# Optimization experiments

Measured on AMD Instinct MI355X. Metric: run time of the kernel, lower is better.

The kernel has to match this reference:

```python
import jax, jax.numpy as jnp
import numpy as np

RADIUS = 0.05
HMIN = -0.02
HMAXES = (0.01, 0.02, 0.03, 0.04)
NSAMPLE = 64
BN_EPS = 1e-5


def _group(d_rot, hmax):
    # d_rot: (B,S,N,3) seed-relative coords rotated into the gripper frame (d @ R)
    # Cylinder query: approach axis is x; keep first NSAMPLE points with
    # y^2+z^2 < r^2 and hmin < x < hmax; pad with first hit (0 if no hit),
    # matching the CUDA cylinder_query kernel semantics.
    N = d_rot.shape[2]
    h = d_rot[..., 0]
    r2 = d_rot[..., 1] ** 2 + d_rot[..., 2] ** 2
    mask = (r2 < RADIUS * RADIUS) & (h > HMIN) & (h < hmax)
    key = jnp.where(mask, jnp.arange(N, dtype=jnp.int32), N)
    neg_top, _ = jax.lax.top_k(-key, NSAMPLE)   # ascending keys = first hits in point order
    idx = -neg_top                               # (B,S,k); == N where slot is invalid
    first = idx[..., :1]
    idx = jnp.where(idx < N, idx, jnp.where(first < N, first, 0))
    return jnp.take_along_axis(d_rot, idx[..., None], axis=2)  # (B,S,k,3)


def _mlp_layer(x, w, b, g, be, m, v):
    # 1x1 Conv2d + BatchNorm (eval-mode, running stats) + ReLU, as in pt_utils.SharedMLP
    x = jnp.einsum('bcpn,oc->bopn', x, w) + b[None, :, None, None]
    scale = g / jnp.sqrt(v + BN_EPS)
    x = (x - m[None, :, None, None]) * scale[None, :, None, None] + be[None, :, None, None]
    return jax.nn.relu(x)


def _forward(seed_xyz, pointcloud, vp_rot, params):
    B, S, _ = seed_xyz.shape
    D = len(HMAXES)
    d = pointcloud[:, None, :, :] - seed_xyz[:, :, None, :]          # (B,S,N,3)
    d_rot = jnp.einsum('bsnc,bscd->bsnd', d, vp_rot)                 # rotate into gripper frame
    groups = jnp.stack([_group(d_rot, h) for h in HMAXES], axis=2)   # (B,S,D,k,3)
    x = groups.transpose(0, 4, 1, 2, 3).reshape(B, 3, S * D, NSAMPLE)  # (B,3,S*D,k)
    for (w, b, g, be, m, v) in params:
        x = _mlp_layer(x, w, b, g, be, m, v)
    x = x.max(axis=-1)                                               # max-pool over nsample
    return x.reshape(B, -1, S, D)                                    # (B,256,S,D)


def setup_inputs() -> dict:
    key = jax.random.key(0)
    ks = jax.random.split(key, 8)
    B, S, N = 2, 1024, 16384
    inp = {
        'seed_xyz': jax.random.uniform(ks[0], (B, S, 3), jnp.float32),
        'pointcloud': jax.random.uniform(ks[1], (B, N, 3), jnp.float32),
        'vp_rot': jax.random.normal(ks[2], (B, S, 3, 3), jnp.float32),
    }
    dims = [3, 64, 128, 256]
    for i in range(3):
        cin, cout = dims[i], dims[i + 1]
        k1, k2, k3, k4, k5, k6 = jax.random.split(ks[3 + i], 6)
        inp[f'w{i+1}'] = jax.random.normal(k1, (cout, cin), jnp.float32) * 0.05
        inp[f'b{i+1}'] = jax.random.normal(k2, (cout,), jnp.float32) * 0.01
        inp[f'g{i+1}'] = 1.0 + 0.1 * jax.random.normal(k3, (cout,), jnp.float32)
        inp[f'be{i+1}'] = jax.random.normal(k4, (cout,), jnp.float32) * 0.01
        inp[f'm{i+1}'] = jax.random.normal(k5, (cout,), jnp.float32) * 0.01
        inp[f'v{i+1}'] = jax.random.uniform(k6, (cout,), jnp.float32, 0.5, 1.5)
    return inp


def reference(seed_xyz, pointcloud, vp_rot,
              w1, b1, g1, be1, m1, v1,
              w2, b2, g2, be2, m2, v2,
              w3, b3, g3, be3, m3, v3):
    params = [(w1, b1, g1, be1, m1, v1),
              (w2, b2, g2, be2, m2, v2),
              (w3, b3, g3, be3, m3, v3)]
    return _forward(seed_xyz, pointcloud, vp_rot, params)
```

## Files before the change

kernel.cpp:

```cpp
#include <hip/hip_runtime.h>
#include <hip/hip_bf16.h>
#include <cstdint>
#include <cstddef>

#define NSAMP  64
#define NPT    16384
#define NLVL   4
#define NCHUNK 8
#define CHSZ   (NPT / NCHUNK)

typedef __attribute__((ext_vector_type(8))) short  short8;
typedef __attribute__((ext_vector_type(4))) float  floatx4;
typedef __attribute__((ext_vector_type(4))) unsigned int uintx4;
typedef __attribute__((ext_vector_type(2))) unsigned int uintx2;

__device__ __forceinline__ unsigned short f2bf(float x) {
    union { float f; unsigned int u; } c; c.f = x;
    unsigned int r = (c.u + 0x7fffu + ((c.u >> 16) & 1u)) >> 16;
    return (unsigned short)r;
}
__device__ __forceinline__ unsigned int f2bf2(float a, float b) {
    __hip_bfloat162 t = __float22bfloat162_rn(make_float2(a, b));
    union { __hip_bfloat162 h; unsigned int u; } c; c.h = t;
    return c.u;
}

__global__ __launch_bounds__(256) void prep_kernel(
    const float* __restrict__ w1, const float* __restrict__ b1, const float* __restrict__ g1,
    const float* __restrict__ be1, const float* __restrict__ m1, const float* __restrict__ v1,
    const float* __restrict__ w2, const float* __restrict__ b2, const float* __restrict__ g2,
    const float* __restrict__ be2, const float* __restrict__ m2, const float* __restrict__ v2,
    const float* __restrict__ w3, const float* __restrict__ b3, const float* __restrict__ g3,
    const float* __restrict__ be3, const float* __restrict__ m3, const float* __restrict__ v3,
    float* __restrict__ w1f, float* __restrict__ fb1,
    unsigned short* __restrict__ w2b, float* __restrict__ fb2,
    unsigned short* __restrict__ w3b, float* __restrict__ fb3)
{
    const int t  = blockIdx.x * 256 + threadIdx.x;
    const int nt = gridDim.x * 256;
    const float eps = 1e-5f;
    for (int i = t; i < 64 * 3; i += nt)    w1f[i] = w1[i] * (g1[i / 3] / sqrtf(v1[i / 3] + eps));
    for (int i = t; i < 64; i += nt)        fb1[i] = (b1[i] - m1[i]) * (g1[i] / sqrtf(v1[i] + eps)) + be1[i];
    for (int i = t; i < 128 * 64; i += nt)  w2b[i] = f2bf(w2[i] * (g2[i / 64] / sqrtf(v2[i / 64] + eps)));
    for (int i = t; i < 128; i += nt)       fb2[i] = (b2[i] - m2[i]) * (g2[i] / sqrtf(v2[i] + eps)) + be2[i];
    for (int i = t; i < 256 * 128; i += nt) w3b[i] = f2bf(w3[i] * (g3[i / 128] / sqrtf(v3[i / 128] + eps)));
    for (int i = t; i < 256; i += nt)       fb3[i] = (b3[i] - m3[i]) * (g3[i] / sqrtf(v3[i] + eps)) + be3[i];
}

__global__ __launch_bounds__(512) void scan_kernel(
    const float* __restrict__ seedp, const float* __restrict__ pc,
    const float* __restrict__ rot, unsigned short* __restrict__ buf,
    int* __restrict__ cnts)
{
    __shared__ float ch[CHSZ * 3];
    const int tid  = threadIdx.x;
    const int lane = tid & 63;
    const int w    = tid >> 6;
    const int sg   = blockIdx.x >> 3;
    const int c    = blockIdx.x & 7;
    const int g    = sg * 8 + w;
    const int b    = g >> 10;

    {
        const float4* src = (const float4*)(pc + ((size_t)b * NPT + c * CHSZ) * 3);
        float4* dst = (float4*)ch;
        dst[tid]        = src[tid];
        dst[tid + 512]  = src[tid + 512];
        dst[tid + 1024] = src[tid + 1024];
    }
    __syncthreads();

    const float* sd = seedp + (size_t)g * 3;
    const float sx = sd[0], sy = sd[1], sz = sd[2];
    const float* R = rot + (size_t)g * 9;
    const float r00 = R[0], r01 = R[1], r02 = R[2];
    const float r10 = R[3], r11 = R[4], r12 = R[5];
    const float r20 = R[6], r21 = R[7], r22 = R[8];
    const float nc0 = -(sx * r00 + sy * r10 + sz * r20);
    const float nc1 = -(sx * r01 + sy * r11 + sz * r21);
    const float nc2 = -(sx * r02 + sy * r12 + sz * r22);

    unsigned short* bufg = buf + (size_t)g * (NLVL * NCHUNK * 64);
    int cnt0 = 0, cnt1 = 0, cnt2 = 0, cnt3 = 0;
    const unsigned long long lm = (1ull << lane) - 1ull;

    for (int bt = 0; bt < 4; ++bt) {
        float pxv[8], pyv[8], pzv[8];
        #pragma unroll
        for (int j = 0; j < 8; ++j) {
            const int pl = (bt * 8 + j) * 64 + lane;
            pxv[j] = ch[pl * 3];
            pyv[j] = ch[pl * 3 + 1];
            pzv[j] = ch[pl * 3 + 2];
        }
        #pragma unroll
        for (int j = 0; j < 8; ++j) {
            const float h = fmaf(pxv[j], r00, fmaf(pyv[j], r10, fmaf(pzv[j], r20, nc0)));
            const float u = fmaf(pxv[j], r01, fmaf(pyv[j], r11, fmaf(pzv[j], r21, nc1)));
            const float v = fmaf(pxv[j], r02, fmaf(pyv[j], r12, fmaf(pzv[j], r22, nc2)));
            const float r2 = fmaf(u, u, v * v);
            const bool base = (r2 < 0.0025f) && (h > -0.02f) && (h < 0.04f);

            const unsigned long long bal3 = __ballot(base);
            if (bal3 == 0ull) continue;

            const unsigned short pidx = (unsigned short)(c * CHSZ + (bt * 8 + j) * 64 + lane);
            #pragma unroll
            for (int l = 0; l < NLVL; ++l) {
                unsigned long long bal; bool m;
                if (l == 3) { m = base; bal = bal3; }
                else {
                    const float hm = (l == 0) ? 0.01f : (l == 1) ? 0.02f : 0.03f;
                    m = base && (h < hm);
                    bal = __ballot(m);
                }
                int& cnt = (l == 0) ? cnt0 : (l == 1) ? cnt1 : (l == 2) ? cnt2 : cnt3;
                if (m) {
                    const int pos = cnt + (int)__popcll(bal & lm);
                    if (pos < 64) bufg[(l * NCHUNK + c) * 64 + pos] = pidx;
                }
                cnt += (int)__popcll(bal);
            }
        }
        if (cnt0 >= NSAMP) break;
    }

    if (lane == 0) {
        int* cg = cnts + (size_t)g * (NLVL * NCHUNK);
        cg[0 * NCHUNK + c] = cnt0;
        cg[1 * NCHUNK + c] = cnt1;
        cg[2 * NCHUNK + c] = cnt2;
        cg[3 * NCHUNK + c] = cnt3;
    }
}

__global__ __launch_bounds__(256) void gather_kernel(
    const float* __restrict__ seedp, const float* __restrict__ pc,
    const float* __restrict__ rot,
    const unsigned short* __restrict__ buf, const int* __restrict__ cnts,
    float* __restrict__ gx)
{
    const int n = threadIdx.x & 63;
    const int W = blockIdx.x * 4 + (threadIdx.x >> 6);
    const int g = W >> 2, l = W & 3;
    const int b = g >> 10;

    const int* cg = cnts + (size_t)g * (NLVL * NCHUNK) + l * NCHUNK;
    const unsigned short* bl = buf + (size_t)g * (NLVL * NCHUNK * 64) + l * (NCHUNK * 64);
    int idx = -1, acc = 0, firstIdx = -1;
    #pragma unroll
    for (int c = 0; c < NCHUNK; ++c) {
        const int cn = min(cg[c], 64);
        if (cn > 0 && firstIdx < 0) firstIdx = (int)bl[c * 64];
        if (n >= acc && n < acc + cn) idx = (int)bl[c * 64 + (n - acc)];
        acc += cn;
    }
    if (idx < 0) idx = (firstIdx >= 0) ? firstIdx : 0;

    const float* sd = seedp + (size_t)g * 3;
    const float* R  = rot   + (size_t)g * 9;
    const float* pp = pc + ((size_t)b * NPT + idx) * 3;
    const float dx = pp[0] - sd[0], dy = pp[1] - sd[1], dz = pp[2] - sd[2];

    float* o = gx + (size_t)W * 192;
    o[n]       = dx * R[0] + dy * R[3] + dz * R[6];
    o[64 + n]  = dx * R[1] + dy * R[4] + dz * R[7];
    o[128 + n] = dx * R[2] + dy * R[5] + dz * R[8];
}

__global__ __launch_bounds__(256) void mlp_kernel(
    const float* __restrict__ gx, const int* __restrict__ cnts,
    const float* __restrict__ w1f, const float* __restrict__ fb1,
    const unsigned short* __restrict__ w2b, const float* __restrict__ fb2,
    const unsigned short* __restrict__ w3b, const float* __restrict__ fb3,
    float* __restrict__ out)
{
    __shared__ unsigned short h1t[4096];
    __shared__ unsigned short h2t[8192];

    const int tid = threadIdx.x;
    const int n      = tid & 63;
    const int w      = tid >> 6;
    const int lane15 = tid & 15;
    const int quad   = (tid & 63) >> 4;

    int fmask;
    {
        const int* cg0 = cnts + (size_t)blockIdx.x * (NLVL * NCHUNK);
        int fm = 0;
        #pragma unroll
        for (int l = 0; l < NLVL; ++l) {
            int kn = 0;
            #pragma unroll
            for (int c = 0; c < NCHUNK; ++c) kn += min(cg0[l * NCHUNK + c], 64);
            fm |= (kn <= 16) ? (1 << l) : 0;
        }
        fmask = __builtin_amdgcn_readfirstlane(fm);
    }

    short8 wa3[4][4];
    float  wb3[4];
    #pragma unroll
    for (int mt = 0; mt < 4; ++mt) {
        const int m0 = (w * 4 + mt) * 16;
        #pragma unroll
        for (int k0 = 0; k0 < 4; ++k0)
            wa3[mt][k0] = *(const short8*)&w3b[(m0 + lane15) * 128 + k0 * 32 + quad * 8];
        wb3[mt] = fb3[m0 + lane15];
    }

    short8 a20[2], a21[2]; floatx4 b2v[2];
    #pragma unroll
    for (int mi = 0; mi < 2; ++mi) {
        const int m0 = (w * 2 + mi) * 16;
        a20[mi] = *(const short8*)&w2b[(m0 + lane15) * 64 + quad * 8];
        a21[mi] = *(const short8*)&w2b[(m0 + lane15) * 64 + 32 + quad * 8];
        b2v[mi] = *(const floatx4*)&fb2[m0 + quad * 4];
    }

    if (fmask == 15) {
        const int gb = blockIdx.x;
        const int b = gb >> 10, s = gb & 1023;

        {
            const float* xb = gx + (size_t)(gb * 4 + (n >> 4)) * 192;
            const int sidx = n & 15;
            const float x0 = xb[sidx], x1 = xb[64 + sidx], x2 = xb[128 + sidx];
            unsigned int p[8];
            #pragma unroll
            for (int j = 0; j < 8; ++j) {
                const int o0 = __builtin_amdgcn_readfirstlane(w * 16 + 2 * j);
                const float a0 = fb1[o0]     + w1f[o0*3]*x0   + w1f[o0*3+1]*x1 + w1f[o0*3+2]*x2;
                const float a1 = fb1[o0 + 1] + w1f[o0*3+3]*x0 + w1f[o0*3+4]*x1 + w1f[o0*3+5]*x2;
                p[j] = f2bf2(fmaxf(a0, 0.f), fmaxf(a1, 0.f));
            }
            *(uintx4*)&h1t[(((w * 2)    ) * 64 + n) * 8] = (uintx4){p[0], p[1], p[2], p[3]};
            *(uintx4*)&h1t[(((w * 2) + 1) * 64 + n) * 8] = (uintx4){p[4], p[5], p[6], p[7]};
        }
        __syncthreads();

        {
            short8 bfr[4][2];
            #pragma unroll
            for (int nt = 0; nt < 4; ++nt)
                #pragma unroll
                for (int k0 = 0; k0 < 2; ++k0)
                    bfr[nt][k0] = *(const short8*)&h1t[((k0 * 4 + quad) * 64 + nt * 16 + lane15) * 8];

            #pragma unroll
            for (int mi = 0; mi < 2; ++mi) {
                const int m0 = (w * 2 + mi) * 16;
                #pragma unroll
                for (int nt = 0; nt < 4; ++nt) {
                    floatx4 acc = b2v[mi];
                    acc = __builtin_amdgcn_mfma_f32_16x16x32_bf16(a20[mi], bfr[nt][0], acc, 0, 0, 0);
                    acc = __builtin_amdgcn_mfma_f32_16x16x32_bf16(a21[mi], bfr[nt][1], acc, 0, 0, 0);
                    const int n2 = nt * 16 + lane15;
                    const unsigned int q0 = f2bf2(fmaxf(acc[0], 0.f), fmaxf(acc[1], 0.f));
                    const unsigned int q1 = f2bf2(fmaxf(acc[2], 0.f), fmaxf(acc[3], 0.f));
                    const int kb = (m0 >> 3) + (quad >> 1);
                    *(uintx2*)&h2t[(kb * 64 + n2) * 8 + (quad & 1) * 4] = (uintx2){q0, q1};
                }
            }
        }
        __syncthreads();

        short8 bfr3[4][4];
        #pragma unroll
        for (int nt = 0; nt < 4; ++nt)
            #pragma unroll
            for (int k0 = 0; k0 < 4; ++k0)
                bfr3[nt][k0] = *(const short8*)&h2t[((k0 * 4 + quad) * 64 + nt * 16 + lane15) * 8];

        #pragma unroll
        for (int mt = 0; mt < 4; ++mt) {
            floatx4 acc[4];
            #pragma unroll
            for (int nt = 0; nt < 4; ++nt) acc[nt] = (floatx4){0.f, 0.f, 0.f, 0.f};
            #pragma unroll
            for (int k0 = 0; k0 < 4; ++k0)
                #pragma unroll
                for (int nt = 0; nt < 4; ++nt)
                    acc[nt] = __builtin_amdgcn_mfma_f32_16x16x32_bf16(bfr3[nt][k0], wa3[mt][k0], acc[nt], 0, 0, 0);

            float tv[4];
            #pragma unroll
            for (int nt = 0; nt < 4; ++nt) {
                float t = fmaxf(fmaxf(acc[nt][0], acc[nt][1]), fmaxf(acc[nt][2], acc[nt][3]));
                t = fmaxf(t, __shfl_xor(t, 16));
                t = fmaxf(t, __shfl_xor(t, 32));
                tv[nt] = fmaxf(t + wb3[mt], 0.f);
            }
            if (quad == 0) {
                const int o = (w * 4 + mt) * 16 + lane15;
                *(float4*)&out[(((size_t)b * 256 + o) * 1024 + s) * 4] =
                    make_float4(tv[0], tv[1], tv[2], tv[3]);
            }
        }
        return;
    }

    {
        const float* xb = gx + (size_t)(blockIdx.x * 4) * 192;
        const float x0 = xb[n], x1 = xb[64 + n], x2 = xb[128 + n];
        unsigned int p[8];
        #pragma unroll
        for (int j = 0; j < 8; ++j) {
            const int o0 = __builtin_amdgcn_readfirstlane(w * 16 + 2 * j);
            const float a0 = fb1[o0]     + w1f[o0*3]*x0   + w1f[o0*3+1]*x1 + w1f[o0*3+2]*x2;
            const float a1 = fb1[o0 + 1] + w1f[o0*3+3]*x0 + w1f[o0*3+4]*x1 + w1f[o0*3+5]*x2;
            p[j] = f2bf2(fmaxf(a0, 0.f), fmaxf(a1, 0.f));
        }
        *(uintx4*)&h1t[(((w * 2)    ) * 64 + n) * 8] = (uintx4){p[0], p[1], p[2], p[3]};
        *(uintx4*)&h1t[(((w * 2) + 1) * 64 + n) * 8] = (uintx4){p[4], p[5], p[6], p[7]};
    }

    for (int it = 0; it < 4; ++it) {
        const int gp = blockIdx.x * 4 + it;
        const int g = gp >> 2, l = gp & 3;
        const int b = g >> 10, s = g & 1023;
        const bool fastit = (fmask >> it) & 1;

        __syncthreads();

        if (fastit) {
            const short8 bA = *(const short8*)&h1t[((0 * 4 + quad) * 64 + lane15) * 8];
            const short8 bB = *(const short8*)&h1t[((1 * 4 + quad) * 64 + lane15) * 8];
            #pragma unroll
            for (int mi = 0; mi < 2; ++mi) {
                floatx4 acc = b2v[mi];
                acc = __builtin_amdgcn_mfma_f32_16x16x32_bf16(a20[mi], bA, acc, 0, 0, 0);
                acc = __builtin_amdgcn_mfma_f32_16x16x32_bf16(a21[mi], bB, acc, 0, 0, 0);
                const unsigned int q0 = f2bf2(fmaxf(acc[0], 0.f), fmaxf(acc[1], 0.f));
                const unsigned int q1 = f2bf2(fmaxf(acc[2], 0.f), fmaxf(acc[3], 0.f));
                const int kb = (w * 2 + mi) * 2 + (quad >> 1);
                *(uintx2*)&h2t[(kb * 64 + lane15) * 8 + (quad & 1) * 4] = (uintx2){q0, q1};
            }
        } else {
            short8 bfr[4][2];
            #pragma unroll
            for (int nt = 0; nt < 4; ++nt)
                #pragma unroll
                for (int k0 = 0; k0 < 2; ++k0)
                    bfr[nt][k0] = *(const short8*)&h1t[((k0 * 4 + quad) * 64 + nt * 16 + lane15) * 8];

            #pragma unroll
            for (int mi = 0; mi < 2; ++mi) {
                const int m0 = (w * 2 + mi) * 16;
                #pragma unroll
                for (int nt = 0; nt < 4; ++nt) {
                    floatx4 acc = b2v[mi];
                    acc = __builtin_amdgcn_mfma_f32_16x16x32_bf16(a20[mi], bfr[nt][0], acc, 0, 0, 0);
                    acc = __builtin_amdgcn_mfma_f32_16x16x32_bf16(a21[mi], bfr[nt][1], acc, 0, 0, 0);
                    const int n2 = nt * 16 + lane15;
                    const unsigned int q0 = f2bf2(fmaxf(acc[0], 0.f), fmaxf(acc[1], 0.f));
                    const unsigned int q1 = f2bf2(fmaxf(acc[2], 0.f), fmaxf(acc[3], 0.f));
                    const int kb = (m0 >> 3) + (quad >> 1);
                    *(uintx2*)&h2t[(kb * 64 + n2) * 8 + (quad & 1) * 4] = (uintx2){q0, q1};
                }
            }
        }
        __syncthreads();

        if (fastit) {
            short8 bf3[4];
            #pragma unroll
            for (int k0 = 0; k0 < 4; ++k0)
                bf3[k0] = *(const short8*)&h2t[((k0 * 4 + quad) * 64 + lane15) * 8];

            if (it < 3) {
                const float* xb = gx + (size_t)(gp + 1) * 192;
                const float x0 = xb[n], x1 = xb[64 + n], x2 = xb[128 + n];
                unsigned int p[8];
                #pragma unroll
                for (int j = 0; j < 8; ++j) {
                    const int o0 = __builtin_amdgcn_readfirstlane(w * 16 + 2 * j);
                    const float a0 = fb1[o0]     + w1f[o0*3]*x0   + w1f[o0*3+1]*x1 + w1f[o0*3+2]*x2;
                    const float a1 = fb1[o0 + 1] + w1f[o0*3+3]*x0 + w1f[o0*3+4]*x1 + w1f[o0*3+5]*x2;
                    p[j] = f2bf2(fmaxf(a0, 0.f), fmaxf(a1, 0.f));
                }
                *(uintx4*)&h1t[(((w * 2)    ) * 64 + n) * 8] = (uintx4){p[0], p[1], p[2], p[3]};
                *(uintx4*)&h1t[(((w * 2) + 1) * 64 + n) * 8] = (uintx4){p[4], p[5], p[6], p[7]};
            }

            #pragma unroll
            for (int mt = 0; mt < 4; ++mt) {
                floatx4 acc = (floatx4){0.f, 0.f, 0.f, 0.f};
                #pragma unroll
                for (int k0 = 0; k0 < 4; ++k0)
                    acc = __builtin_amdgcn_mfma_f32_16x16x32_bf16(bf3[k0], wa3[mt][k0], acc, 0, 0, 0);

                float t = fmaxf(fmaxf(acc[0], acc[1]), fmaxf(acc[2], acc[3]));
                t = fmaxf(t, __shfl_xor(t, 16));
                t = fmaxf(t, __shfl_xor(t, 32));
                if (quad == 0) {
                    const int o = (w * 4 + mt) * 16 + lane15;
                    out[(((size_t)b * 256 + o) * 1024 + s) * 4 + l] = fmaxf(t + wb3[mt], 0.f);
                }
            }
        } else {
            short8 bfr3[4][4];
            #pragma unroll
            for (int nt = 0; nt < 4; ++nt)
                #pragma unroll
                for (int k0 = 0; k0 < 4; ++k0)
                    bfr3[nt][k0] = *(const short8*)&h2t[((k0 * 4 + quad) * 64 + nt * 16 + lane15) * 8];

            if (it < 3) {
                const float* xb = gx + (size_t)(gp + 1) * 192;
                const float x0 = xb[n], x1 = xb[64 + n], x2 = xb[128 + n];
                unsigned int p[8];
                #pragma unroll
                for (int j = 0; j < 8; ++j) {
                    const int o0 = __builtin_amdgcn_readfirstlane(w * 16 + 2 * j);
                    const float a0 = fb1[o0]     + w1f[o0*3]*x0   + w1f[o0*3+1]*x1 + w1f[o0*3+2]*x2;
                    const float a1 = fb1[o0 + 1] + w1f[o0*3+3]*x0 + w1f[o0*3+4]*x1 + w1f[o0*3+5]*x2;
                    p[j] = f2bf2(fmaxf(a0, 0.f), fmaxf(a1, 0.f));
                }
                *(uintx4*)&h1t[(((w * 2)    ) * 64 + n) * 8] = (uintx4){p[0], p[1], p[2], p[3]};
                *(uintx4*)&h1t[(((w * 2) + 1) * 64 + n) * 8] = (uintx4){p[4], p[5], p[6], p[7]};
            }

            #pragma unroll
            for (int mt = 0; mt < 4; ++mt) {
                floatx4 acc[4];
                #pragma unroll
                for (int nt = 0; nt < 4; ++nt) acc[nt] = (floatx4){0.f, 0.f, 0.f, 0.f};
                #pragma unroll
                for (int k0 = 0; k0 < 4; ++k0)
                    #pragma unroll
                    for (int nt = 0; nt < 4; ++nt)
                        acc[nt] = __builtin_amdgcn_mfma_f32_16x16x32_bf16(bfr3[nt][k0], wa3[mt][k0], acc[nt], 0, 0, 0);

                float t0 = fmaxf(fmaxf(acc[0][0], acc[0][1]), fmaxf(acc[0][2], acc[0][3]));
                float t1 = fmaxf(fmaxf(acc[1][0], acc[1][1]), fmaxf(acc[1][2], acc[1][3]));
                float t2 = fmaxf(fmaxf(acc[2][0], acc[2][1]), fmaxf(acc[2][2], acc[2][3]));
                float t3 = fmaxf(fmaxf(acc[3][0], acc[3][1]), fmaxf(acc[3][2], acc[3][3]));
                float t  = fmaxf(fmaxf(t0, t1), fmaxf(t2, t3));
                t = fmaxf(t, __shfl_xor(t, 16));
                t = fmaxf(t, __shfl_xor(t, 32));
                if (quad == 0) {
                    const int o = (w * 4 + mt) * 16 + lane15;
                    out[(((size_t)b * 256 + o) * 1024 + s) * 4 + l] = fmaxf(t + wb3[mt], 0.f);
                }
            }
        }
    }
}

extern "C" void kernel_launch(void* const* d_in, const int* in_sizes, int n_in,
                              void* d_out, int out_size, void* d_ws, size_t ws_size,
                              hipStream_t stream) {
    const float* seed = (const float*)d_in[0];
    const float* pc   = (const float*)d_in[1];
    const float* rot  = (const float*)d_in[2];
    const float* w1 = (const float*)d_in[3];
    const float* b1 = (const float*)d_in[4];
    const float* g1 = (const float*)d_in[5];
    const float* be1 = (const float*)d_in[6];
    const float* m1 = (const float*)d_in[7];
    const float* v1 = (const float*)d_in[8];
    const float* w2 = (const float*)d_in[9];
    const float* b2 = (const float*)d_in[10];
    const float* g2 = (const float*)d_in[11];
    const float* be2 = (const float*)d_in[12];
    const float* m2 = (const float*)d_in[13];
    const float* v2 = (const float*)d_in[14];
    const float* w3 = (const float*)d_in[15];
    const float* b3 = (const float*)d_in[16];
    const float* g3 = (const float*)d_in[17];
    const float* be3 = (const float*)d_in[18];
    const float* m3 = (const float*)d_in[19];
    const float* v3 = (const float*)d_in[20];

    float* w1f = (float*)d_ws;
    float* fb1 = w1f + 192;
    float* fb2 = fb1 + 64;
    float* fb3 = fb2 + 128;
    unsigned short* w2b = (unsigned short*)(fb3 + 256);
    unsigned short* w3b = w2b + 8192;
    unsigned short* buf = w3b + 32768;
    int* cnts = (int*)(buf + 4194304);
    float* gx = (float*)(cnts + 65536);

    prep_kernel<<<64, 256, 0, stream>>>(w1, b1, g1, be1, m1, v1,
                                        w2, b2, g2, be2, m2, v2,
                                        w3, b3, g3, be3, m3, v3,
                                        w1f, fb1, w2b, fb2, w3b, fb3);
    scan_kernel<<<2048, 512, 0, stream>>>(seed, pc, rot, buf, cnts);
    gather_kernel<<<2048, 256, 0, stream>>>(seed, pc, rot, buf, cnts, gx);
    mlp_kernel<<<2048, 256, 0, stream>>>(gx, cnts, w1f, fb1, w2b, fb2, w3b, fb3,
                                         (float*)d_out);
}
```

Baseline: 168.5 us.

## Fold weight prep into scan kernel and split MLP work by group occupancy

Measured after the change: 177.3 us. +5.2%, slower.

```diff
diff --git a/kernel.cpp b/kernel.cpp
--- a/kernel.cpp
+++ b/kernel.cpp
@@ -25,7 +25,10 @@
     return c.u;
 }
 
-__global__ __launch_bounds__(256) void prep_kernel(
+__global__ __launch_bounds__(512) void scan_kernel(
+    const float* __restrict__ seedp, const float* __restrict__ pc,
+    const float* __restrict__ rot, unsigned short* __restrict__ buf,
+    int* __restrict__ cnts,
     const float* __restrict__ w1, const float* __restrict__ b1, const float* __restrict__ g1,
     const float* __restrict__ be1, const float* __restrict__ m1, const float* __restrict__ v1,
     const float* __restrict__ w2, const float* __restrict__ b2, const float* __restrict__ g2,
@@ -36,24 +39,22 @@
     unsigned short* __restrict__ w2b, float* __restrict__ fb2,
     unsigned short* __restrict__ w3b, float* __restrict__ fb3)
 {
-    const int t  = blockIdx.x * 256 + threadIdx.x;
-    const int nt = gridDim.x * 256;
-    const float eps = 1e-5f;
-    for (int i = t; i < 64 * 3; i += nt)    w1f[i] = w1[i] * (g1[i / 3] / sqrtf(v1[i / 3] + eps));
-    for (int i = t; i < 64; i += nt)        fb1[i] = (b1[i] - m1[i]) * (g1[i] / sqrtf(v1[i] + eps)) + be1[i];
-    for (int i = t; i < 128 * 64; i += nt)  w2b[i] = f2bf(w2[i] * (g2[i / 64] / sqrtf(v2[i / 64] + eps)));
-    for (int i = t; i < 128; i += nt)       fb2[i] = (b2[i] - m2[i]) * (g2[i] / sqrtf(v2[i] + eps)) + be2[i];
-    for (int i = t; i < 256 * 128; i += nt) w3b[i] = f2bf(w3[i] * (g3[i / 128] / sqrtf(v3[i / 128] + eps)));
-    for (int i = t; i < 256; i += nt)       fb3[i] = (b3[i] - m3[i]) * (g3[i] / sqrtf(v3[i] + eps)) + be3[i];
-}
-
-__global__ __launch_bounds__(512) void scan_kernel(
-    const float* __restrict__ seedp, const float* __restrict__ pc,
-    const float* __restrict__ rot, unsigned short* __restrict__ buf,
-    int* __restrict__ cnts)
-{
     __shared__ float ch[CHSZ * 3];
     const int tid  = threadIdx.x;
+
+    if (blockIdx.x >= 2048) {
+        const int t  = (blockIdx.x - 2048) * 512 + tid;
+        const int nt = 64 * 512;
+        const float eps = 1e-5f;
+        for (int i = t; i < 64 * 3; i += nt)    w1f[i] = w1[i] * (g1[i / 3] / sqrtf(v1[i / 3] + eps));
+        for (int i = t; i < 64; i += nt)        fb1[i] = (b1[i] - m1[i]) * (g1[i] / sqrtf(v1[i] + eps)) + be1[i];
+        for (int i = t; i < 128 * 64; i += nt)  w2b[i] = f2bf(w2[i] * (g2[i / 64] / sqrtf(v2[i / 64] + eps)));
+        for (int i = t; i < 128; i += nt)       fb2[i] = (b2[i] - m2[i]) * (g2[i] / sqrtf(v2[i] + eps)) + be2[i];
+        for (int i = t; i < 256 * 128; i += nt) w3b[i] = f2bf(w3[i] * (g3[i / 128] / sqrtf(v3[i / 128] + eps)));
+        for (int i = t; i < 256; i += nt)       fb3[i] = (b3[i] - m3[i]) * (g3[i] / sqrtf(v3[i] + eps)) + be3[i];
+        return;
+    }
+
     const int lane = tid & 63;
     const int w    = tid >> 6;
     const int sg   = blockIdx.x >> 3;
@@ -184,48 +185,42 @@
     const int lane15 = tid & 15;
     const int quad   = (tid & 63) >> 4;
 
-    int fmask;
-    {
-        const int* cg0 = cnts + (size_t)blockIdx.x * (NLVL * NCHUNK);
-        int fm = 0;
-        #pragma unroll
-        for (int l = 0; l < NLVL; ++l) {
+    const int bi = blockIdx.x;
+
+    if (bi < 8192) {
+        const int gp = bi;
+        const int g = gp >> 2, l = gp & 3;
+        {
+            const int* cg = cnts + (size_t)g * (NLVL * NCHUNK) + l * NCHUNK;
             int kn = 0;
             #pragma unroll
-            for (int c = 0; c < NCHUNK; ++c) kn += min(cg0[l * NCHUNK + c], 64);
-            fm |= (kn <= 16) ? (1 << l) : 0;
-        }
-        fmask = __builtin_amdgcn_readfirstlane(fm);
-    }
-
-    short8 wa3[4][4];
-    float  wb3[4];
-    #pragma unroll
-    for (int mt = 0; mt < 4; ++mt) {
-        const int m0 = (w * 4 + mt) * 16;
-        #pragma unroll
-        for (int k0 = 0; k0 < 4; ++k0)
-            wa3[mt][k0] = *(const short8*)&w3b[(m0 + lane15) * 128 + k0 * 32 + quad * 8];
-        wb3[mt] = fb3[m0 + lane15];
-    }
-
-    short8 a20[2], a21[2]; floatx4 b2v[2];
-    #pragma unroll
-    for (int mi = 0; mi < 2; ++mi) {
-        const int m0 = (w * 2 + mi) * 16;
-        a20[mi] = *(const short8*)&w2b[(m0 + lane15) * 64 + quad * 8];
-        a21[mi] = *(const short8*)&w2b[(m0 + lane15) * 64 + 32 + quad * 8];
-        b2v[mi] = *(const floatx4*)&fb2[m0 + quad * 4];
-    }
-
-    if (fmask == 15) {
-        const int gb = blockIdx.x;
-        const int b = gb >> 10, s = gb & 1023;
+            for (int c = 0; c < NCHUNK; ++c) kn += min(cg[c], 64);
+            if (__builtin_amdgcn_readfirstlane(kn) <= 16) return;
+        }
+        const int b = g >> 10, s = g & 1023;
+
+        short8 wa3[4][4];
+        float  wb3[4];
+        #pragma unroll
+        for (int mt = 0; mt < 4; ++mt) {
+            const int m0 = (w * 4 + mt) * 16;
+            #pragma unroll
+            for (int k0 = 0; k0 < 4; ++k0)
+                wa3[mt][k0] = *(const short8*)&w3b[(m0 + lane15) * 128 + k0 * 32 + quad * 8];
+            wb3[mt] = fb3[m0 + lane15];
+        }
+        short8 a20[2], a21[2]; floatx4 b2v[2];
+        #pragma unroll
+        for (int mi = 0; mi < 2; ++mi) {
+            const int m0 = (w * 2 + mi) * 16;
+            a20[mi] = *(const short8*)&w2b[(m0 + lane15) * 64 + quad * 8];
+            a21[mi] = *(const short8*)&w2b[(m0 + lane15) * 64 + 32 + quad * 8];
+            b2v[mi] = *(const floatx4*)&fb2[m0 + quad * 4];
+        }
 
         {
-            const float* xb = gx + (size_t)(gb * 4 + (n >> 4)) * 192;
-            const int sidx = n & 15;
-            const float x0 = xb[sidx], x1 = xb[64 + sidx], x2 = xb[128 + sidx];
+            const float* xb = gx + (size_t)gp * 192;
+            const float x0 = xb[n], x1 = xb[64 + n], x2 = xb[128 + n];
             unsigned int p[8];
             #pragma unroll
             for (int j = 0; j < 8; ++j) {
@@ -283,26 +278,63 @@
                 for (int nt = 0; nt < 4; ++nt)
                     acc[nt] = __builtin_amdgcn_mfma_f32_16x16x32_bf16(bfr3[nt][k0], wa3[mt][k0], acc[nt], 0, 0, 0);
 
-            float tv[4];
-            #pragma unroll
-            for (int nt = 0; nt < 4; ++nt) {
-                float t = fmaxf(fmaxf(acc[nt][0], acc[nt][1]), fmaxf(acc[nt][2], acc[nt][3]));
-                t = fmaxf(t, __shfl_xor(t, 16));
-                t = fmaxf(t, __shfl_xor(t, 32));
-                tv[nt] = fmaxf(t + wb3[mt], 0.f);
-            }
+            float t0 = fmaxf(fmaxf(acc[0][0], acc[0][1]), fmaxf(acc[0][2], acc[0][3]));
+            float t1 = fmaxf(fmaxf(acc[1][0], acc[1][1]), fmaxf(acc[1][2], acc[1][3]));
+            float t2 = fmaxf(fmaxf(acc[2][0], acc[2][1]), fmaxf(acc[2][2], acc[2][3]));
+            float t3 = fmaxf(fmaxf(acc[3][0], acc[3][1]), fmaxf(acc[3][2], acc[3][3]));
+            float t  = fmaxf(fmaxf(t0, t1), fmaxf(t2, t3));
+            t = fmaxf(t, __shfl_xor(t, 16));
+            t = fmaxf(t, __shfl_xor(t, 32));
             if (quad == 0) {
                 const int o = (w * 4 + mt) * 16 + lane15;
-                *(float4*)&out[(((size_t)b * 256 + o) * 1024 + s) * 4] =
-                    make_float4(tv[0], tv[1], tv[2], tv[3]);
+                out[(((size_t)b * 256 + o) * 1024 + s) * 4 + l] = fmaxf(t + wb3[mt], 0.f);
             }
         }
         return;
     }
 
+    const int gb = bi - 8192;
+    const int b = gb >> 10, s = gb & 1023;
+
+    int F;
     {
-        const float* xb = gx + (size_t)(blockIdx.x * 4) * 192;
-        const float x0 = xb[n], x1 = xb[64 + n], x2 = xb[128 + n];
+        const int* cg0 = cnts + (size_t)gb * (NLVL * NCHUNK);
+        int fm = 0;
+        #pragma unroll
+        for (int l = 0; l < NLVL; ++l) {
+            int kn = 0;
+            #pragma unroll
+            for (int c = 0; c < NCHUNK; ++c) kn += min(cg0[l * NCHUNK + c], 64);
+            fm += (kn <= 16) ? 1 : 0;
+        }
+        F = __builtin_amdgcn_readfirstlane(fm);
+    }
+    if (F == 0) return;
+
+    short8 wa3[4][4];
+    float  wb3[4];
+    #pragma unroll
+    for (int mt = 0; mt < 4; ++mt) {
+        const int m0 = (w * 4 + mt) * 16;
+        #pragma unroll
+        for (int k0 = 0; k0 < 4; ++k0)
+            wa3[mt][k0] = *(const short8*)&w3b[(m0 + lane15) * 128 + k0 * 32 + quad * 8];
+        wb3[mt] = fb3[m0 + lane15];
+    }
+    short8 a20[2], a21[2]; floatx4 b2v[2];
+    #pragma unroll
+    for (int mi = 0; mi < 2; ++mi) {
+        const int m0 = (w * 2 + mi) * 16;
+        a20[mi] = *(const short8*)&w2b[(m0 + lane15) * 64 + quad * 8];
+        a21[mi] = *(const short8*)&w2b[(m0 + lane15) * 64 + 32 + quad * 8];
+        b2v[mi] = *(const floatx4*)&fb2[m0 + quad * 4];
+    }
+
+    {
+        const int lvl = min(n >> 4, F - 1);
+        const float* xb = gx + (size_t)(gb * 4 + lvl) * 192;
+        const int sidx = n & 15;
+        const float x0 = xb[sidx], x1 = xb[64 + sidx], x2 = xb[128 + sidx];
         unsigned int p[8];
         #pragma unroll
         for (int j = 0; j < 8; ++j) {
@@ -314,135 +346,69 @@
         *(uintx4*)&h1t[(((w * 2)    ) * 64 + n) * 8] = (uintx4){p[0], p[1], p[2], p[3]};
         *(uintx4*)&h1t[(((w * 2) + 1) * 64 + n) * 8] = (uintx4){p[4], p[5], p[6], p[7]};
     }
-
-    for (int it = 0; it < 4; ++it) {
-        const int gp = blockIdx.x * 4 + it;
-        const int g = gp >> 2, l = gp & 3;
-        const int b = g >> 10, s = g & 1023;
-        const bool fastit = (fmask >> it) & 1;
-
-        __syncthreads();
-
-        if (fastit) {
-            const short8 bA = *(const short8*)&h1t[((0 * 4 + quad) * 64 + lane15) * 8];
-            const short8 bB = *(const short8*)&h1t[((1 * 4 + quad) * 64 + lane15) * 8];
-            #pragma unroll
-            for (int mi = 0; mi < 2; ++mi) {
+    __syncthreads();
+
+    {
+        short8 bfr[4][2];
+        #pragma unroll
+        for (int nt = 0; nt < 4; ++nt)
+            #pragma unroll
+            for (int k0 = 0; k0 < 2; ++k0)
+                bfr[nt][k0] = *(const short8*)&h1t[((k0 * 4 + quad) * 64 + nt * 16 + lane15) * 8];
+
+        #pragma unroll
+        for (int mi = 0; mi < 2; ++mi) {
+            const int m0 = (w * 2 + mi) * 16;
+            #pragma unroll
+            for (int nt = 0; nt < 4; ++nt) {
                 floatx4 acc = b2v[mi];
-                acc = __builtin_amdgcn_mfma_f32_16x16x32_bf16(a20[mi], bA, acc, 0, 0, 0);
-                acc = __builtin_amdgcn_mfma_f32_16x16x32_bf16(a21[mi], bB, acc, 0, 0, 0);
+                acc = __builtin_amdgcn_mfma_f32_16x16x32_bf16(a20[mi], bfr[nt][0], acc, 0, 0, 0);
+                acc = __builtin_amdgcn_mfma_f32_16x16x32_bf16(a21[mi], bfr[nt][1], acc, 0, 0, 0);
+                const int n2 = nt * 16 + lane15;
                 const unsigned int q0 = f2bf2(fmaxf(acc[0], 0.f), fmaxf(acc[1], 0.f));
                 const unsigned int q1 = f2bf2(fmaxf(acc[2], 0.f), fmaxf(acc[3], 0.f));
-                const int kb = (w * 2 + mi) * 2 + (quad >> 1);
-                *(uintx2*)&h2t[(kb * 64 + lane15) * 8 + (quad & 1) * 4] = (uintx2){q0, q1};
-            }
-        } else {
-            short8 bfr[4][2];
+                const int kb = (m0 >> 3) + (quad >> 1);
+                *(uintx2*)&h2t[(kb * 64 + n2) * 8 + (quad & 1) * 4] = (uintx2){q0, q1};
+            }
+        }
+    }
+    __syncthreads();
+
+    short8 bfr3[4][4];
+    #pragma unroll
+    for (int nt = 0; nt < 4; ++nt)
+        #pragma unroll
+        for (int k0 = 0; k0 < 4; ++k0)
+            bfr3[nt][k0] = *(const short8*)&h2t[((k0 * 4 + quad) * 64 + nt * 16 + lane15) * 8];
+
+    #pragma unroll
+    for (int mt = 0; mt < 4; ++mt) {
+        floatx4 acc[4];
+        #pragma unroll
+        for (int nt = 0; nt < 4; ++nt) acc[nt] = (floatx4){0.f, 0.f, 0.f, 0.f};
+        #pragma unroll
+        for (int k0 = 0; k0 < 4; ++k0)
             #pragma unroll
             for (int nt = 0; nt < 4; ++nt)
-                #pragma unroll
-                for (int k0 = 0; k0 < 2; ++k0)
-                    bfr[nt][k0] = *(const short8*)&h1t[((k0 * 4 + quad) * 64 + nt * 16 + lane15) * 8];
-
-            #pragma unroll
-            for (int mi = 0; mi < 2; ++mi) {
-                const int m0 = (w * 2 + mi) * 16;
-                #pragma unroll
-                for (int nt = 0; nt < 4; ++nt) {
-                    floatx4 acc = b2v[mi];
-                    acc = __builtin_amdgcn_mfma_f32_16x16x32_bf16(a20[mi], bfr[nt][0], acc, 0, 0, 0);
-                    acc = __builtin_amdgcn_mfma_f32_16x16x32_bf16(a21[mi], bfr[nt][1], acc, 0, 0, 0);
-                    const int n2 = nt * 16 + lane15;
-                    const unsigned int q0 = f2bf2(fmaxf(acc[0], 0.f), fmaxf(acc[1], 0.f));
-                    const unsigned int q1 = f2bf2(fmaxf(acc[2], 0.f), fmaxf(acc[3], 0.f));
-                    const int kb = (m0 >> 3) + (quad >> 1);
-                    *(uintx2*)&h2t[(kb * 64 + n2) * 8 + (quad & 1) * 4] = (uintx2){q0, q1};
-                }
-            }
-        }
-        __syncthreads();
-
-        if (fastit) {
-            short8 bf3[4];
-            #pragma unroll
-            for (int k0 = 0; k0 < 4; ++k0)
-                bf3[k0] = *(const short8*)&h2t[((k0 * 4 + quad) * 64 + lane15) * 8];
-
-            if (it < 3) {
-                const float* xb = gx + (size_t)(gp + 1) * 192;
-                const float x0 = xb[n], x1 = xb[64 + n], x2 = xb[128 + n];
-                unsigned int p[8];
-                #pragma unroll
-                for (int j = 0; j < 8; ++j) {
-                    const int o0 = __builtin_amdgcn_readfirstlane(w * 16 + 2 * j);
-                    const float a0 = fb1[o0]     + w1f[o0*3]*x0   + w1f[o0*3+1]*x1 + w1f[o0*3+2]*x2;
-                    const float a1 = fb1[o0 + 1] + w1f[o0*3+3]*x0 + w1f[o0*3+4]*x1 + w1f[o0*3+5]*x2;
-                    p[j] = f2bf2(fmaxf(a0, 0.f), fmaxf(a1, 0.f));
-                }
-                *(uintx4*)&h1t[(((w * 2)    ) * 64 + n) * 8] = (uintx4){p[0], p[1], p[2], p[3]};
-                *(uintx4*)&h1t[(((w * 2) + 1) * 64 + n) * 8] = (uintx4){p[4], p[5], p[6], p[7]};
-            }
-
-            #pragma unroll
-            for (int mt = 0; mt < 4; ++mt) {
-                floatx4 acc = (floatx4){0.f, 0.f, 0.f, 0.f};
-                #pragma unroll
-                for (int k0 = 0; k0 < 4; ++k0)
-                    acc = __builtin_amdgcn_mfma_f32_16x16x32_bf16(bf3[k0], wa3[mt][k0], acc, 0, 0, 0);
-
-                float t = fmaxf(fmaxf(acc[0], acc[1]), fmaxf(acc[2], acc[3]));
-                t = fmaxf(t, __shfl_xor(t, 16));
-                t = fmaxf(t, __shfl_xor(t, 32));
-                if (quad == 0) {
-                    const int o = (w * 4 + mt) * 16 + lane15;
-                    out[(((size_t)b * 256 + o) * 1024 + s) * 4 + l] = fmaxf(t + wb3[mt], 0.f);
-                }
-            }
-        } else {
-            short8 bfr3[4][4];
-            #pragma unroll
-            for (int nt = 0; nt < 4; ++nt)
-                #pragma unroll
-                for (int k0 = 0; k0 < 4; ++k0)
-                    bfr3[nt][k0] = *(const short8*)&h2t[((k0 * 4 + quad) * 64 + nt * 16 + lane15) * 8];
-
-            if (it < 3) {
-                const float* xb = gx + (size_t)(gp + 1) * 192;
-                const float x0 = xb[n], x1 = xb[64 + n], x2 = xb[128 + n];
-                unsigned int p[8];
-                #pragma unroll
-                for (int j = 0; j < 8; ++j) {
-                    const int o0 = __builtin_amdgcn_readfirstlane(w * 16 + 2 * j);
-                    const float a0 = fb1[o0]     + w1f[o0*3]*x0   + w1f[o0*3+1]*x1 + w1f[o0*3+2]*x2;
-                    const float a1 = fb1[o0 + 1] + w1f[o0*3+3]*x0 + w1f[o0*3+4]*x1 + w1f[o0*3+5]*x2;
-                    p[j] = f2bf2(fmaxf(a0, 0.f), fmaxf(a1, 0.f));
-                }
-                *(uintx4*)&h1t[(((w * 2)    ) * 64 + n) * 8] = (uintx4){p[0], p[1], p[2], p[3]};
-                *(uintx4*)&h1t[(((w * 2) + 1) * 64 + n) * 8] = (uintx4){p[4], p[5], p[6], p[7]};
-            }
-
-            #pragma unroll
-            for (int mt = 0; mt < 4; ++mt) {
-                floatx4 acc[4];
-                #pragma unroll
-                for (int nt = 0; nt < 4; ++nt) acc[nt] = (floatx4){0.f, 0.f, 0.f, 0.f};
-                #pragma unroll
-                for (int k0 = 0; k0 < 4; ++k0)
-                    #pragma unroll
-                    for (int nt = 0; nt < 4; ++nt)
-                        acc[nt] = __builtin_amdgcn_mfma_f32_16x16x32_bf16(bfr3[nt][k0], wa3[mt][k0], acc[nt], 0, 0, 0);
-
-                float t0 = fmaxf(fmaxf(acc[0][0], acc[0][1]), fmaxf(acc[0][2], acc[0][3]));
-                float t1 = fmaxf(fmaxf(acc[1][0], acc[1][1]), fmaxf(acc[1][2], acc[1][3]));
-                float t2 = fmaxf(fmaxf(acc[2][0], acc[2][1]), fmaxf(acc[2][2], acc[2][3]));
-                float t3 = fmaxf(fmaxf(acc[3][0], acc[3][1]), fmaxf(acc[3][2], acc[3][3]));
-                float t  = fmaxf(fmaxf(t0, t1), fmaxf(t2, t3));
-                t = fmaxf(t, __shfl_xor(t, 16));
-                t = fmaxf(t, __shfl_xor(t, 32));
-                if (quad == 0) {
-                    const int o = (w * 4 + mt) * 16 + lane15;
-                    out[(((size_t)b * 256 + o) * 1024 + s) * 4 + l] = fmaxf(t + wb3[mt], 0.f);
-                }
+                acc[nt] = __builtin_amdgcn_mfma_f32_16x16x32_bf16(bfr3[nt][k0], wa3[mt][k0], acc[nt], 0, 0, 0);
+
+        float tv[4];
+        #pragma unroll
+        for (int nt = 0; nt < 4; ++nt) {
+            float t = fmaxf(fmaxf(acc[nt][0], acc[nt][1]), fmaxf(acc[nt][2], acc[nt][3]));
+            t = fmaxf(t, __shfl_xor(t, 16));
+            t = fmaxf(t, __shfl_xor(t, 32));
+            tv[nt] = fmaxf(t + wb3[mt], 0.f);
+        }
+        if (quad == 0) {
+            const int o = (w * 4 + mt) * 16 + lane15;
+            float* op = &out[(((size_t)b * 256 + o) * 1024 + s) * 4];
+            if (F == 4) {
+                *(float4*)op = make_float4(tv[0], tv[1], tv[2], tv[3]);
+            } else {
+                op[0] = tv[0];
+                if (F > 1) op[1] = tv[1];
+                if (F > 2) op[2] = tv[2];
             }
         }
     }
@@ -483,12 +449,12 @@
     int* cnts = (int*)(buf + 4194304);
     float* gx = (float*)(cnts + 65536);
 
-    prep_kernel<<<64, 256, 0, stream>>>(w1, b1, g1, be1, m1, v1,
-                                        w2, b2, g2, be2, m2, v2,
-                                        w3, b3, g3, be3, m3, v3,
-                                        w1f, fb1, w2b, fb2, w3b, fb3);
-    scan_kernel<<<2048, 512, 0, stream>>>(seed, pc, rot, buf, cnts);
+    scan_kernel<<<2112, 512, 0, stream>>>(seed, pc, rot, buf, cnts,
+                                          w1, b1, g1, be1, m1, v1,
+                                          w2, b2, g2, be2, m2, v2,
+                                          w3, b3, g3, be3, m3, v3,
+                                          w1f, fb1, w2b, fb2, w3b, fb3);
     gather_kernel<<<2048, 256, 0, stream>>>(seed, pc, rot, buf, cnts, gx);
-    mlp_kernel<<<2048, 256, 0, stream>>>(gx, cnts, w1f, fb1, w2b, fb2, w3b, fb3,
-                                         (float*)d_out);
-}
+    mlp_kernel<<<10240, 256, 0, stream>>>(gx, cnts, w1f, fb1, w2b, fb2, w3b, fb3,
+                                          (float*)d_out);
+}
```
